# Kernel optimization log

Hardware: AMD Instinct MI355X
Metric: run time of the kernel (lower is better)

## Reference

```python
import jax, jax.numpy as jnp
import numpy as np

BIT = 64
M_MARGIN = 2.0 * BIT  # m = 2 * bit
ALPHA = 0.1
N_TRAIN = 100000
N_CLASSES = 100
BATCH = 512


def setup_inputs() -> dict:
    key = jax.random.key(0)
    k1, k2, k3, k4 = jax.random.split(key, 4)
    u = jax.random.normal(k1, (BATCH, BIT), dtype=jnp.float32)
    y = jax.random.randint(k2, (BATCH, N_CLASSES), 0, 2).astype(jnp.float32)
    ind = jnp.arange(BATCH, dtype=jnp.int32)
    U = jax.random.normal(k3, (N_TRAIN, BIT), dtype=jnp.float32)
    Y = jax.random.randint(k4, (N_TRAIN, N_CLASSES), 0, 2).astype(jnp.float32)
    return {"u": u, "y": y, "ind": ind, "U": U, "Y": Y}


def reference(u, y, ind, U, Y):
    # Buffer updates (torch uses u.data / y.float(): detached writes)
    U = U.at[ind].set(jax.lax.stop_gradient(u))  # [N, bit]
    Y = Y.at[ind].set(jax.lax.stop_gradient(y))  # [N, C]

    # Pairwise squared L2 distances via the expansion identity (same math as
    # (u[:,None]-U[None]).pow(2).sum(-1) but without the [B,N,bit] intermediate)
    u_sq = jnp.sum(u * u, axis=1, keepdims=True)        # [B, 1]
    U_sq = jnp.sum(U * U, axis=1)[None, :]              # [1, N]
    dist = jnp.maximum(u_sq - 2.0 * (u @ U.T) + U_sq, 0.0)  # [B, N]

    # match mask: 1 where labels share no class (y @ Y.T == 0)
    mismatch = (y @ Y.T == 0).astype(u.dtype)           # [B, N]

    loss = (1.0 - mismatch) * 0.5 * dist + mismatch * 0.5 * jnp.maximum(M_MARGIN - dist, 0.0)
    loss1 = loss.mean()
    loss2 = ALPHA * jnp.abs(1.0 - jnp.sign(u)).mean()
    return loss1 + loss2
```

## Files before the change

### kernel.cpp

```cpp
#include <hip/hip_runtime.h>
#include <stdint.h>

#define NTRAIN 100000
#define BATCH  512
#define BIT    64
#define NCLS   100
#define MARGINF 128.0f

#define YMASK_OFF   0
#define YMASK_BYTES (NTRAIN * 16)
#define SMASK_OFF   YMASK_BYTES
#define SMASK_BYTES (BATCH * 16)
#define ACC_OFF     (YMASK_BYTES + SMASK_BYTES)

__global__ void k_scatter_init(const float* __restrict__ u, const float* __restrict__ y,
                               const int* __restrict__ ind,
                               float* __restrict__ U, float* __restrict__ Y,
                               float* __restrict__ accf) {
  int bid = blockIdx.x, t = threadIdx.x;
  if (bid < BATCH) {
    int n = ind[bid];
    if (t < BIT)  U[(size_t)n * BIT  + t] = u[bid * BIT  + t];
    if (t < NCLS) Y[(size_t)n * NCLS + t] = y[bid * NCLS + t];
  } else {
    for (int i = t; i < 144; i += blockDim.x) accf[i] = 0.0f;
  }
}

__device__ __forceinline__ uint4 row_mask(const float* __restrict__ row) {
  const float4* r4 = (const float4*)row;
  unsigned w0 = 0, w1 = 0, w2 = 0, w3 = 0;
#pragma unroll
  for (int j = 0; j < NCLS / 4; ++j) {
    float4 v = r4[j];
    int bp = (4 * j) & 31;
    unsigned m = ((v.x != 0.f) ? 1u : 0u) << bp
               | ((v.y != 0.f) ? 2u : 0u) << bp
               | ((v.z != 0.f) ? 4u : 0u) << bp
               | ((v.w != 0.f) ? 8u : 0u) << bp;
    int word = (4 * j) >> 5;
    if (word == 0) w0 |= m; else if (word == 1) w1 |= m;
    else if (word == 2) w2 |= m; else w3 |= m;
  }
  return make_uint4(w0, w1, w2, w3);
}

#define U_BLKS   256
#define YM_BLKS  512
#define SM_BLKS  2
#define US_BLKS  2

__global__ void __launch_bounds__(256) k_stats(
    const float4* __restrict__ U4, const float* __restrict__ Y,
    const float4* __restrict__ u4, const float* __restrict__ y,
    uint4* __restrict__ Ymask, uint4* __restrict__ ymaskp,
    float* __restrict__ accf) {
  int bid = blockIdx.x, t = threadIdx.x;
  int w = t >> 6, l = t & 63;

  if (bid < U_BLKS) {
    const int TOT = U_BLKS * 256;
    int tid = bid * 256 + t;
    float s0 = 0, s1 = 0, s2 = 0, s3 = 0, sq = 0;
    for (int f = tid; f < NTRAIN * (BIT / 4); f += TOT) {
      float4 v = U4[f];
      s0 += v.x; s1 += v.y; s2 += v.z; s3 += v.w;
      sq = fmaf(v.x, v.x, fmaf(v.y, v.y, fmaf(v.z, v.z, fmaf(v.w, v.w, sq))));
    }
    s0 += __shfl_xor(s0, 16); s0 += __shfl_xor(s0, 32);
    s1 += __shfl_xor(s1, 16); s1 += __shfl_xor(s1, 32);
    s2 += __shfl_xor(s2, 16); s2 += __shfl_xor(s2, 32);
    s3 += __shfl_xor(s3, 16); s3 += __shfl_xor(s3, 32);
    for (int off = 32; off; off >>= 1) sq += __shfl_xor(sq, off);
    __shared__ float cols[4][64];
    __shared__ float sqs[4];
    if (l < 16) { cols[w][l * 4 + 0] = s0; cols[w][l * 4 + 1] = s1;
                  cols[w][l * 4 + 2] = s2; cols[w][l * 4 + 3] = s3; }
    if (l == 0) sqs[w] = sq;
    __syncthreads();
    if (w == 0) {
      atomicAdd(&accf[l], cols[0][l] + cols[1][l] + cols[2][l] + cols[3][l]);
      if (l == 0) atomicAdd(&accf[128], sqs[0] + sqs[1] + sqs[2] + sqs[3]);
    }
  } else if (bid < U_BLKS + YM_BLKS) {
    int n = (bid - U_BLKS) * 256 + t;
    if (n < NTRAIN) Ymask[n] = row_mask(Y + (size_t)n * NCLS);
  } else if (bid < U_BLKS + YM_BLKS + SM_BLKS) {
    int b = (bid - U_BLKS - YM_BLKS) * 256 + t;
    if (b < BATCH) ymaskp[b] = row_mask(y + (size_t)b * NCLS);
  } else {
    int tid = (bid - U_BLKS - YM_BLKS - SM_BLKS) * 256 + t;
    const int TOT = US_BLKS * 256;
    float s0 = 0, s1 = 0, s2 = 0, s3 = 0, sq = 0, sg = 0;
    for (int f = tid; f < BATCH * (BIT / 4); f += TOT) {
      float4 v = u4[f];
      s0 += v.x; s1 += v.y; s2 += v.z; s3 += v.w;
      sq = fmaf(v.x, v.x, fmaf(v.y, v.y, fmaf(v.z, v.z, fmaf(v.w, v.w, sq))));
      sg += ((v.x < 0.f) ? 2.f : (v.x == 0.f) ? 1.f : 0.f)
          + ((v.y < 0.f) ? 2.f : (v.y == 0.f) ? 1.f : 0.f)
          + ((v.z < 0.f) ? 2.f : (v.z == 0.f) ? 1.f : 0.f)
          + ((v.w < 0.f) ? 2.f : (v.w == 0.f) ? 1.f : 0.f);
    }
    s0 += __shfl_xor(s0, 16); s0 += __shfl_xor(s0, 32);
    s1 += __shfl_xor(s1, 16); s1 += __shfl_xor(s1, 32);
    s2 += __shfl_xor(s2, 16); s2 += __shfl_xor(s2, 32);
    s3 += __shfl_xor(s3, 16); s3 += __shfl_xor(s3, 32);
    for (int off = 32; off; off >>= 1) { sq += __shfl_xor(sq, off); sg += __shfl_xor(sg, off); }
    int c4 = l & 15;
    if (l < 16) {
      atomicAdd(&accf[64 + c4 * 4 + 0], s0);
      atomicAdd(&accf[64 + c4 * 4 + 1], s1);
      atomicAdd(&accf[64 + c4 * 4 + 2], s2);
      atomicAdd(&accf[64 + c4 * 4 + 3], s3);
    }
    if (l == 0) { atomicAdd(&accf[129], sq); atomicAdd(&accf[130], sg); }
  }
}

#define NCHUNK 64

__global__ void __launch_bounds__(512) k_scan(
    const uint4* __restrict__ Ymask, const uint4* __restrict__ ymaskp,
    const float* __restrict__ u, const float* __restrict__ U,
    float* __restrict__ accf) {
  int b = threadIdx.x;
  uint4 ym = ymaskp[b];
  int n0 = blockIdx.x * NCHUNK;
  int nend = n0 + NCHUNK; if (nend > NTRAIN) nend = NTRAIN;
  float corr = 0.f;
  for (int n = n0; n < nend; ++n) {
    uint4 Ym = Ymask[n];
    unsigned m = (ym.x & Ym.x) | (ym.y & Ym.y) | (ym.z & Ym.z) | (ym.w & Ym.w);
    if (__builtin_expect(__ballot(m == 0u) != 0ull, 0)) {
      if (m == 0u) {
        const float4* ub = (const float4*)(u + (size_t)b * BIT);
        const float4* Un = (const float4*)(U + (size_t)n * BIT);
        float usq = 0.f, Usq = 0.f, uv = 0.f;
        for (int k = 0; k < BIT / 4; ++k) {
          float4 a = ub[k], c = Un[k];
          usq = fmaf(a.x, a.x, fmaf(a.y, a.y, fmaf(a.z, a.z, fmaf(a.w, a.w, usq))));
          Usq = fmaf(c.x, c.x, fmaf(c.y, c.y, fmaf(c.z, c.z, fmaf(c.w, c.w, Usq))));
          uv  = fmaf(a.x, c.x, fmaf(a.y, c.y, fmaf(a.z, c.z, fmaf(a.w, c.w, uv))));
        }
        float d = usq + Usq - 2.f * uv;
        float dc = fmaxf(d, 0.f);
        corr += 0.5f * fmaxf(MARGINF - dc, 0.f) - 0.5f * d;
      }
    }
  }
  if (corr != 0.f) atomicAdd(&accf[131], corr);
}

__global__ void k_final(const float* __restrict__ accf, float* __restrict__ out) {
  int lane = threadIdx.x;
  double dotp = (double)accf[lane] * (double)accf[64 + lane];
  for (int off = 32; off; off >>= 1) dotp += __shfl_down(dotp, off);
  if (lane == 0) {
    double S_Usq = accf[128];
    double s_usq = accf[129];
    double sg    = accf[130];
    double corr  = accf[131];
    double sum_dist = (double)NTRAIN * s_usq + (double)BATCH * S_Usq - 2.0 * dotp;
    double loss1 = (0.5 * sum_dist + corr) / ((double)BATCH * (double)NTRAIN);
    double loss2 = 0.1 * sg / ((double)BATCH * (double)BIT);
    out[0] = (float)(loss1 + loss2);
  }
}

extern "C" void kernel_launch(void* const* d_in, const int* in_sizes, int n_in,
                              void* d_out, int out_size, void* d_ws, size_t ws_size,
                              hipStream_t stream) {
  const float* u   = (const float*)d_in[0];
  const float* y   = (const float*)d_in[1];
  const int*   ind = (const int*)d_in[2];
  float* U = (float*)d_in[3];
  float* Y = (float*)d_in[4];
  uint4* Ymask  = (uint4*)((char*)d_ws + YMASK_OFF);
  uint4* ymaskp = (uint4*)((char*)d_ws + SMASK_OFF);
  float* accf   = (float*)((char*)d_ws + ACC_OFF);
  float* out    = (float*)d_out;

  hipLaunchKernelGGL(k_scatter_init, dim3(BATCH + 1), dim3(128), 0, stream,
                     u, y, ind, U, Y, accf);
  hipLaunchKernelGGL(k_stats, dim3(U_BLKS + YM_BLKS + SM_BLKS + US_BLKS), dim3(256), 0, stream,
                     (const float4*)U, Y, (const float4*)u, y, Ymask, ymaskp, accf);
  hipLaunchKernelGGL(k_scan, dim3((NTRAIN + NCHUNK - 1) / NCHUNK), dim3(512), 0, stream,
                     Ymask, ymaskp, u, U, accf);
  hipLaunchKernelGGL(k_final, dim3(1), dim3(64), 0, stream, accf, out);
}
```

Before: 131.8 us.

## Drop scatter, fuse mask build and stats into scan with batch-row corrections

Removes the in-place scatter of u/y into the U/Y buffers. The stale batch rows are instead handled algebraically: their contributions to the column sums and squared norms are subtracted, and the pair terms for old versus new labels are corrected in dedicated blocks. The Y mask is built per chunk into shared memory inside the main scan kernel, fusing the stats, mask and scan kernels and avoiding a global mask round trip. This cuts launches and global traffic, but the input buffers are no longer updated and the correction assumes indices in ind are unique.

```diff
diff --git a/kernel.cpp b/kernel.cpp
--- a/kernel.cpp
+++ b/kernel.cpp
@@ -7,25 +7,12 @@
 #define NCLS   100
 #define MARGINF 128.0f
 
-#define YMASK_OFF   0
-#define YMASK_BYTES (NTRAIN * 16)
-#define SMASK_OFF   YMASK_BYTES
-#define SMASK_BYTES (BATCH * 16)
-#define ACC_OFF     (YMASK_BYTES + SMASK_BYTES)
-
-__global__ void k_scatter_init(const float* __restrict__ u, const float* __restrict__ y,
-                               const int* __restrict__ ind,
-                               float* __restrict__ U, float* __restrict__ Y,
-                               float* __restrict__ accf) {
-  int bid = blockIdx.x, t = threadIdx.x;
-  if (bid < BATCH) {
-    int n = ind[bid];
-    if (t < BIT)  U[(size_t)n * BIT  + t] = u[bid * BIT  + t];
-    if (t < NCLS) Y[(size_t)n * NCLS + t] = y[bid * NCLS + t];
-  } else {
-    for (int i = t; i < 144; i += blockDim.x) accf[i] = 0.0f;
-  }
-}
+#define CHUNK  256
+#define NSCAN  ((NTRAIN + CHUNK - 1) / CHUNK)
+#define NCORR  8
+#define NGU    2
+#define NUS    2
+
 
 __device__ __forceinline__ uint4 row_mask(const float* __restrict__ row) {
   const float4* r4 = (const float4*)row;
@@ -45,25 +32,62 @@
   return make_uint4(w0, w1, w2, w3);
 }
 
-#define U_BLKS   256
-#define YM_BLKS  512
-#define SM_BLKS  2
-#define US_BLKS  2
-
-__global__ void __launch_bounds__(256) k_stats(
-    const float4* __restrict__ U4, const float* __restrict__ Y,
-    const float4* __restrict__ u4, const float* __restrict__ y,
-    uint4* __restrict__ Ymask, uint4* __restrict__ ymaskp,
+__device__ __forceinline__ float pair_term(const float* __restrict__ a,
+                                           const float* __restrict__ c) {
+  const float4* a4 = (const float4*)a;
+  const float4* c4 = (const float4*)c;
+  float usq = 0.f, Usq = 0.f, uv = 0.f;
+#pragma unroll
+  for (int k = 0; k < BIT / 4; ++k) {
+    float4 x = a4[k], z = c4[k];
+    usq = fmaf(x.x, x.x, fmaf(x.y, x.y, fmaf(x.z, x.z, fmaf(x.w, x.w, usq))));
+    Usq = fmaf(z.x, z.x, fmaf(z.y, z.y, fmaf(z.z, z.z, fmaf(z.w, z.w, Usq))));
+    uv  = fmaf(x.x, z.x, fmaf(x.y, z.y, fmaf(x.z, z.z, fmaf(x.w, z.w, uv))));
+  }
+  float d = usq + Usq - 2.f * uv;
+  float dc = fmaxf(d, 0.f);
+  return 0.5f * fmaxf(MARGINF - dc, 0.f) - 0.5f * d;
+}
+
+__global__ void __launch_bounds__(64) k_prep(const float* __restrict__ y,
+                                             const float* __restrict__ Y,
+                                             const int* __restrict__ ind,
+                                             uint4* __restrict__ ymaskp,
+                                             uint4* __restrict__ ymold,
+                                             float* __restrict__ accf) {
+  int bid = blockIdx.x, t = threadIdx.x;
+  if (bid < 8) {
+    int b = bid * 64 + t;
+    ymaskp[b] = row_mask(y + (size_t)b * NCLS);
+    ymold[b]  = row_mask(Y + (size_t)ind[b] * NCLS);
+  } else {
+    for (int i = t; i < 144; i += 64) accf[i] = 0.0f;
+  }
+}
+
+__global__ void __launch_bounds__(512) k_main(
+    const float4* __restrict__ U4, const float* __restrict__ Uf,
+    const float* __restrict__ Y,
+    const float4* __restrict__ u4, const float* __restrict__ u,
+    const int* __restrict__ ind,
+    const uint4* __restrict__ ymaskp, const uint4* __restrict__ ymold,
     float* __restrict__ accf) {
+  __shared__ uint4 masks[CHUNK];
+  __shared__ float colred[8][64];
+  __shared__ float sqred[8][2];
   int bid = blockIdx.x, t = threadIdx.x;
   int w = t >> 6, l = t & 63;
 
-  if (bid < U_BLKS) {
-    const int TOT = U_BLKS * 256;
-    int tid = bid * 256 + t;
+  if (bid < NSCAN) {
+    uint4 ym = ymaskp[t];
+    int n0 = bid * CHUNK;
+    int nvalid = min(CHUNK, NTRAIN - n0);
+    if (t < CHUNK)
+      masks[t] = (t < nvalid) ? row_mask(Y + (size_t)(n0 + t) * NCLS)
+                              : make_uint4(~0u, ~0u, ~0u, ~0u);
     float s0 = 0, s1 = 0, s2 = 0, s3 = 0, sq = 0;
-    for (int f = tid; f < NTRAIN * (BIT / 4); f += TOT) {
-      float4 v = U4[f];
+    for (int f = t; f < nvalid * (BIT / 4); f += 512) {
+      float4 v = U4[(size_t)n0 * (BIT / 4) + f];
       s0 += v.x; s1 += v.y; s2 += v.z; s3 += v.w;
       sq = fmaf(v.x, v.x, fmaf(v.y, v.y, fmaf(v.z, v.z, fmaf(v.w, v.w, sq))));
     }
@@ -72,28 +96,80 @@
     s2 += __shfl_xor(s2, 16); s2 += __shfl_xor(s2, 32);
     s3 += __shfl_xor(s3, 16); s3 += __shfl_xor(s3, 32);
     for (int off = 32; off; off >>= 1) sq += __shfl_xor(sq, off);
-    __shared__ float cols[4][64];
-    __shared__ float sqs[4];
-    if (l < 16) { cols[w][l * 4 + 0] = s0; cols[w][l * 4 + 1] = s1;
-                  cols[w][l * 4 + 2] = s2; cols[w][l * 4 + 3] = s3; }
-    if (l == 0) sqs[w] = sq;
+    if (l < 16) { colred[w][l * 4 + 0] = s0; colred[w][l * 4 + 1] = s1;
+                  colred[w][l * 4 + 2] = s2; colred[w][l * 4 + 3] = s3; }
+    if (l == 0) sqred[w][0] = sq;
     __syncthreads();
     if (w == 0) {
-      atomicAdd(&accf[l], cols[0][l] + cols[1][l] + cols[2][l] + cols[3][l]);
-      if (l == 0) atomicAdd(&accf[128], sqs[0] + sqs[1] + sqs[2] + sqs[3]);
-    }
-  } else if (bid < U_BLKS + YM_BLKS) {
-    int n = (bid - U_BLKS) * 256 + t;
-    if (n < NTRAIN) Ymask[n] = row_mask(Y + (size_t)n * NCLS);
-  } else if (bid < U_BLKS + YM_BLKS + SM_BLKS) {
-    int b = (bid - U_BLKS - YM_BLKS) * 256 + t;
-    if (b < BATCH) ymaskp[b] = row_mask(y + (size_t)b * NCLS);
+      float cs = 0;
+#pragma unroll
+      for (int ww = 0; ww < 8; ++ww) cs += colred[ww][l];
+      atomicAdd(&accf[l], cs);
+      if (l == 0) {
+        float qs = 0;
+#pragma unroll
+        for (int ww = 0; ww < 8; ++ww) qs += sqred[ww][0];
+        atomicAdd(&accf[128], qs);
+      }
+    }
+    float corr = 0.f;
+    for (int j = 0; j < CHUNK; j += 4) {
+      uint4 m0 = masks[j], m1 = masks[j + 1], m2 = masks[j + 2], m3 = masks[j + 3];
+      unsigned a0 = (ym.x & m0.x) | (ym.y & m0.y) | (ym.z & m0.z) | (ym.w & m0.w);
+      unsigned a1 = (ym.x & m1.x) | (ym.y & m1.y) | (ym.z & m1.z) | (ym.w & m1.w);
+      unsigned a2 = (ym.x & m2.x) | (ym.y & m2.y) | (ym.z & m2.z) | (ym.w & m2.w);
+      unsigned a3 = (ym.x & m3.x) | (ym.y & m3.y) | (ym.z & m3.z) | (ym.w & m3.w);
+      if (__builtin_expect((a0 == 0u) | (a1 == 0u) | (a2 == 0u) | (a3 == 0u), 0)) {
+        const float* ub = u + (size_t)t * BIT;
+        if (a0 == 0u) corr += pair_term(ub, Uf + (size_t)(n0 + j + 0) * BIT);
+        if (a1 == 0u) corr += pair_term(ub, Uf + (size_t)(n0 + j + 1) * BIT);
+        if (a2 == 0u) corr += pair_term(ub, Uf + (size_t)(n0 + j + 2) * BIT);
+        if (a3 == 0u) corr += pair_term(ub, Uf + (size_t)(n0 + j + 3) * BIT);
+      }
+    }
+    if (corr != 0.f) atomicAdd(&accf[131], corr);
+  } else if (bid < NSCAN + NCORR) {
+    int cb = bid - NSCAN;
+    uint4 ym = ymaskp[t];
+    float corr = 0.f;
+    for (int j = 0; j < 64; ++j) {
+      int bp = cb * 64 + j;
+      uint4 mo = ymold[bp];
+      uint4 mn = ymaskp[bp];
+      unsigned a = (ym.x & mo.x) | (ym.y & mo.y) | (ym.z & mo.z) | (ym.w & mo.w);
+      unsigned c = (ym.x & mn.x) | (ym.y & mn.y) | (ym.z & mn.z) | (ym.w & mn.w);
+      if (__builtin_expect(__ballot((a == 0u) | (c == 0u)) != 0ull, 0)) {
+        const float* ub = u + (size_t)t * BIT;
+        if (a == 0u) corr -= pair_term(ub, Uf + (size_t)ind[bp] * BIT);
+        if (c == 0u) corr += pair_term(ub, u + (size_t)bp * BIT);
+      }
+    }
+    if (corr != 0.f) atomicAdd(&accf[131], corr);
+  } else if (bid < NSCAN + NCORR + NGU) {
+    int gb = bid - NSCAN - NCORR;
+    float s0 = 0, s1 = 0, s2 = 0, s3 = 0, sq = 0;
+    for (int f = t; f < 256 * (BIT / 4); f += 512) {
+      int r = gb * 256 + (f >> 4);
+      float4 v = U4[(size_t)ind[r] * (BIT / 4) + (f & 15)];
+      s0 += v.x; s1 += v.y; s2 += v.z; s3 += v.w;
+      sq = fmaf(v.x, v.x, fmaf(v.y, v.y, fmaf(v.z, v.z, fmaf(v.w, v.w, sq))));
+    }
+    s0 += __shfl_xor(s0, 16); s0 += __shfl_xor(s0, 32);
+    s1 += __shfl_xor(s1, 16); s1 += __shfl_xor(s1, 32);
+    s2 += __shfl_xor(s2, 16); s2 += __shfl_xor(s2, 32);
+    s3 += __shfl_xor(s3, 16); s3 += __shfl_xor(s3, 32);
+    for (int off = 32; off; off >>= 1) sq += __shfl_xor(sq, off);
+    int c4 = l & 15;
+    if (l < 16) {
+      atomicAdd(&accf[c4 * 4 + 0], -s0); atomicAdd(&accf[c4 * 4 + 1], -s1);
+      atomicAdd(&accf[c4 * 4 + 2], -s2); atomicAdd(&accf[c4 * 4 + 3], -s3);
+    }
+    if (l == 0) atomicAdd(&accf[128], -sq);
   } else {
-    int tid = (bid - U_BLKS - YM_BLKS - SM_BLKS) * 256 + t;
-    const int TOT = US_BLKS * 256;
+    int gb = bid - NSCAN - NCORR - NGU;
     float s0 = 0, s1 = 0, s2 = 0, s3 = 0, sq = 0, sg = 0;
-    for (int f = tid; f < BATCH * (BIT / 4); f += TOT) {
-      float4 v = u4[f];
+    for (int f = t; f < 256 * (BIT / 4); f += 512) {
+      float4 v = u4[(size_t)gb * 256 * (BIT / 4) + f];
       s0 += v.x; s1 += v.y; s2 += v.z; s3 += v.w;
       sq = fmaf(v.x, v.x, fmaf(v.y, v.y, fmaf(v.z, v.z, fmaf(v.w, v.w, sq))));
       sg += ((v.x < 0.f) ? 2.f : (v.x == 0.f) ? 1.f : 0.f)
@@ -108,47 +184,11 @@
     for (int off = 32; off; off >>= 1) { sq += __shfl_xor(sq, off); sg += __shfl_xor(sg, off); }
     int c4 = l & 15;
     if (l < 16) {
-      atomicAdd(&accf[64 + c4 * 4 + 0], s0);
-      atomicAdd(&accf[64 + c4 * 4 + 1], s1);
-      atomicAdd(&accf[64 + c4 * 4 + 2], s2);
-      atomicAdd(&accf[64 + c4 * 4 + 3], s3);
+      atomicAdd(&accf[64 + c4 * 4 + 0], s0); atomicAdd(&accf[64 + c4 * 4 + 1], s1);
+      atomicAdd(&accf[64 + c4 * 4 + 2], s2); atomicAdd(&accf[64 + c4 * 4 + 3], s3);
     }
     if (l == 0) { atomicAdd(&accf[129], sq); atomicAdd(&accf[130], sg); }
   }
-}
-
-#define NCHUNK 64
-
-__global__ void __launch_bounds__(512) k_scan(
-    const uint4* __restrict__ Ymask, const uint4* __restrict__ ymaskp,
-    const float* __restrict__ u, const float* __restrict__ U,
-    float* __restrict__ accf) {
-  int b = threadIdx.x;
-  uint4 ym = ymaskp[b];
-  int n0 = blockIdx.x * NCHUNK;
-  int nend = n0 + NCHUNK; if (nend > NTRAIN) nend = NTRAIN;
-  float corr = 0.f;
-  for (int n = n0; n < nend; ++n) {
-    uint4 Ym = Ymask[n];
-    unsigned m = (ym.x & Ym.x) | (ym.y & Ym.y) | (ym.z & Ym.z) | (ym.w & Ym.w);
-    if (__builtin_expect(__ballot(m == 0u) != 0ull, 0)) {
-      if (m == 0u) {
-        const float4* ub = (const float4*)(u + (size_t)b * BIT);
-        const float4* Un = (const float4*)(U + (size_t)n * BIT);
-        float usq = 0.f, Usq = 0.f, uv = 0.f;
-        for (int k = 0; k < BIT / 4; ++k) {
-          float4 a = ub[k], c = Un[k];
-          usq = fmaf(a.x, a.x, fmaf(a.y, a.y, fmaf(a.z, a.z, fmaf(a.w, a.w, usq))));
-          Usq = fmaf(c.x, c.x, fmaf(c.y, c.y, fmaf(c.z, c.z, fmaf(c.w, c.w, Usq))));
-          uv  = fmaf(a.x, c.x, fmaf(a.y, c.y, fmaf(a.z, c.z, fmaf(a.w, c.w, uv))));
-        }
-        float d = usq + Usq - 2.f * uv;
-        float dc = fmaxf(d, 0.f);
-        corr += 0.5f * fmaxf(MARGINF - dc, 0.f) - 0.5f * d;
-      }
-    }
-  }
-  if (corr != 0.f) atomicAdd(&accf[131], corr);
 }
 
 __global__ void k_final(const float* __restrict__ accf, float* __restrict__ out) {
@@ -173,18 +213,15 @@
   const float* u   = (const float*)d_in[0];
   const float* y   = (const float*)d_in[1];
   const int*   ind = (const int*)d_in[2];
-  float* U = (float*)d_in[3];
-  float* Y = (float*)d_in[4];
-  uint4* Ymask  = (uint4*)((char*)d_ws + YMASK_OFF);
-  uint4* ymaskp = (uint4*)((char*)d_ws + SMASK_OFF);
-  float* accf   = (float*)((char*)d_ws + ACC_OFF);
+  const float* U   = (const float*)d_in[3];
+  const float* Y   = (const float*)d_in[4];
+  uint4* ymaskp = (uint4*)((char*)d_ws);
+  uint4* ymold  = (uint4*)((char*)d_ws + 8192);
+  float* accf   = (float*)((char*)d_ws + 16384);
   float* out    = (float*)d_out;
 
-  hipLaunchKernelGGL(k_scatter_init, dim3(BATCH + 1), dim3(128), 0, stream,
-                     u, y, ind, U, Y, accf);
-  hipLaunchKernelGGL(k_stats, dim3(U_BLKS + YM_BLKS + SM_BLKS + US_BLKS), dim3(256), 0, stream,
-                     (const float4*)U, Y, (const float4*)u, y, Ymask, ymaskp, accf);
-  hipLaunchKernelGGL(k_scan, dim3((NTRAIN + NCHUNK - 1) / NCHUNK), dim3(512), 0, stream,
-                     Ymask, ymaskp, u, U, accf);
+  hipLaunchKernelGGL(k_prep, dim3(9), dim3(64), 0, stream, y, Y, ind, ymaskp, ymold, accf);
+  hipLaunchKernelGGL(k_main, dim3(NSCAN + NCORR + NGU + NUS), dim3(512), 0, stream,
+                     (const float4*)U, U, Y, (const float4*)u, u, ind, ymaskp, ymold, accf);
   hipLaunchKernelGGL(k_final, dim3(1), dim3(64), 0, stream, accf, out);
 }
```

New measurement: 129.6 us. No clear change (-1.7%).
